# Kernel optimization log

Measured on AMD Instinct MI355X. Metric: run time of the kernel, lower is better.

Reference implementation:

```python
import jax, jax.numpy as jnp
import numpy as np

NUM_HEAD = 8


def setup_inputs() -> dict:
    key = jax.random.key(0)
    ks = jax.random.split(key, 8)
    B, N, M, C, R = 4, 2048, 2048, 256, 128
    s = 1.0 / np.sqrt(C)
    return {
        "input_q": jax.random.normal(ks[0], (B, N, C), jnp.float32),
        "input_k": jax.random.normal(ks[1], (B, M, C), jnp.float32),
        "input_v": jax.random.normal(ks[2], (B, M, C), jnp.float32),
        "rpe_indices": jax.random.randint(ks[3], (B, N, M), 0, R, jnp.int32),
        "key_masks": jnp.zeros((B, M), jnp.float32),
        "Wq": jax.random.normal(ks[4], (C, C), jnp.float32) * s,
        "bq": jnp.zeros((C,), jnp.float32),
        "Wk": jax.random.normal(ks[5], (C, C), jnp.float32) * s,
        "bk": jnp.zeros((C,), jnp.float32),
        "Wv": jax.random.normal(ks[6], (C, C), jnp.float32) * s,
        "bv": jnp.zeros((C,), jnp.float32),
        "rpe_bank": jax.random.normal(ks[7], (R, C), jnp.float32),
    }


def reference(input_q, input_k, input_v, rpe_indices, key_masks,
              Wq, bq, Wk, bk, Wv, bv, rpe_bank):
    B, N, C = input_q.shape
    M = input_k.shape[1]
    H = NUM_HEAD
    Dh = C // H
    R = rpe_bank.shape[0]

    # projections -> (B, H, len, Dh)
    q = (input_q @ Wq + bq).reshape(B, N, H, Dh).transpose(0, 2, 1, 3)
    k = (input_k @ Wk + bk).reshape(B, M, H, Dh).transpose(0, 2, 1, 3)
    v = (input_v @ Wv + bv).reshape(B, M, H, Dh).transpose(0, 2, 1, 3)

    # RPE bank split per head: (H, R, Dh)
    rpe = rpe_bank.reshape(R, H, Dh).transpose(1, 0, 2)

    # q . rpe for all bins, then gather per (n, m) relative index
    scores_p_all = jnp.einsum('bhnd,hrd->bhnr', q, rpe)            # (B,H,N,R)
    idx = jnp.broadcast_to(rpe_indices[:, None, :, :], (B, H, N, M))
    scores_p = jnp.take_along_axis(scores_p_all, idx, axis=-1)     # (B,H,N,M)

    scores_e = jnp.einsum('bhnd,bhmd->bhnm', q, k)                 # (B,H,N,M)
    scores = (scores_e + scores_p) / jnp.sqrt(jnp.asarray(Dh, q.dtype))
    scores = scores + key_masks[:, None, None, :]

    attn = jax.nn.softmax(scores, axis=-1)
    out = jnp.einsum('bhnm,bhmd->bhnd', attn, v)                   # (B,H,N,Dh)
    return out.transpose(0, 2, 1, 3).reshape(B, N, C)
```

## Files before the change

kernel.cpp:

```cpp
#include <hip/hip_runtime.h>
#include <hip/hip_bf16.h>

#define B_ 4
#define N_ 2048
#define M_ 2048
#define C_ 256
#define H_ 8
#define DH_ 32
#define R_ 128

typedef __bf16 bf16x8 __attribute__((ext_vector_type(8)));
typedef float f32x4 __attribute__((ext_vector_type(4)));

__global__ __launch_bounds__(256) void wtrans_kernel(
    const float* __restrict__ Wq, const float* __restrict__ Wk,
    const float* __restrict__ Wv, __bf16* __restrict__ out)
{
    __shared__ float t[32][33];
    int pz = blockIdx.z;
    const float* W = pz == 0 ? Wq : (pz == 1 ? Wk : Wv);
    int j0 = blockIdx.x * 32, k0 = blockIdx.y * 32;
    int tx = threadIdx.x, ty = threadIdx.y;
#pragma unroll
    for (int i = 0; i < 4; ++i)
        t[ty + 8 * i][tx] = W[(k0 + ty + 8 * i) * C_ + j0 + tx];
    __syncthreads();
    __bf16* o = out + (size_t)pz * C_ * C_;
#pragma unroll
    for (int i = 0; i < 4; ++i)
        o[(j0 + ty + 8 * i) * C_ + k0 + tx] = (__bf16)t[tx][ty + 8 * i];
}

__global__ __launch_bounds__(256) void proj_kernel(
    const float* __restrict__ Xq, const float* __restrict__ Xk, const float* __restrict__ Xv,
    const float* __restrict__ bq, const float* __restrict__ bk, const float* __restrict__ bv,
    const __bf16* __restrict__ Wt,
    __bf16* __restrict__ qb, __bf16* __restrict__ kb, __bf16* __restrict__ vt)
{
    int pz = blockIdx.z;
    const float* X = pz == 0 ? Xq : (pz == 1 ? Xk : Xv);
    const float* bias = pz == 0 ? bq : (pz == 1 ? bk : bv);
    const __bf16* W = Wt + (size_t)pz * C_ * C_;

    int r0 = blockIdx.x * 64, c0 = blockIdx.y * 64;
    int w = threadIdx.x >> 6, lane = threadIdx.x & 63;
    int lg = lane >> 4, lr = lane & 15;
    int rw = r0 + w * 16;

    f32x4 z = {0.f, 0.f, 0.f, 0.f};
    f32x4 acc[4] = {z, z, z, z};

    for (int ks = 0; ks < 8; ++ks) {
        const float* ap = X + (size_t)(rw + lr) * C_ + ks * 32 + lg * 8;
        float4 a0 = *(const float4*)ap;
        float4 a1 = *(const float4*)(ap + 4);
        bf16x8 af;
        af[0] = (__bf16)a0.x; af[1] = (__bf16)a0.y; af[2] = (__bf16)a0.z; af[3] = (__bf16)a0.w;
        af[4] = (__bf16)a1.x; af[5] = (__bf16)a1.y; af[6] = (__bf16)a1.z; af[7] = (__bf16)a1.w;
#pragma unroll
        for (int ns = 0; ns < 4; ++ns) {
            bf16x8 bfv = *(const bf16x8*)(W + (size_t)(c0 + ns * 16 + lr) * C_ + ks * 32 + lg * 8);
            acc[ns] = __builtin_amdgcn_mfma_f32_16x16x32_bf16(af, bfv, acc[ns], 0, 0, 0);
        }
    }

#pragma unroll
    for (int ns = 0; ns < 4; ++ns) {
        int j = c0 + ns * 16 + lr;
        float bj = bias[j];
        int h = j >> 5, d = j & 31;
#pragma unroll
        for (int reg = 0; reg < 4; ++reg) {
            int r = rw + lg * 4 + reg;
            int bb = r >> 11, n = r & (N_ - 1);
            float val = acc[ns][reg] + bj;
            if (pz == 0)
                qb[(((size_t)bb * H_ + h) * N_ + n) * DH_ + d] = (__bf16)val;
            else if (pz == 1)
                kb[(((size_t)bb * H_ + h) * M_ + n) * DH_ + d] = (__bf16)val;
            else
                vt[(((size_t)bb * H_ + h) * DH_ + d) * M_ + n] = (__bf16)val;
        }
    }
}

__global__ __launch_bounds__(512) void attn_kernel(
    const __bf16* __restrict__ qb, const __bf16* __restrict__ kb,
    const __bf16* __restrict__ vt, const int* __restrict__ ridx,
    const float* __restrict__ kmask, const float* __restrict__ rbank,
    float* __restrict__ out)
{
    __shared__ int idxS[16][66];
    __shared__ __bf16 Pall[H_][16][R_];
    __shared__ __bf16 Pt[H_][1024];

    int b = blockIdx.y;
    int n0 = blockIdx.x * 16;
    int h = threadIdx.x >> 6, lane = threadIdx.x & 63;
    int lg = lane >> 4, lr = lane & 15;

    f32x4 z = {0.f, 0.f, 0.f, 0.f};

    bf16x8 qf = *(const bf16x8*)(qb + (((size_t)b * H_ + h) * N_ + n0 + lr) * DH_ + lg * 8);

    for (int rs = 0; rs < R_ / 16; ++rs) {
        const float* rp = rbank + (size_t)(rs * 16 + lr) * C_ + h * DH_ + lg * 8;
        float4 r0v = *(const float4*)rp;
        float4 r1v = *(const float4*)(rp + 4);
        bf16x8 rf;
        rf[0] = (__bf16)r0v.x; rf[1] = (__bf16)r0v.y; rf[2] = (__bf16)r0v.z; rf[3] = (__bf16)r0v.w;
        rf[4] = (__bf16)r1v.x; rf[5] = (__bf16)r1v.y; rf[6] = (__bf16)r1v.z; rf[7] = (__bf16)r1v.w;
        f32x4 pc = __builtin_amdgcn_mfma_f32_16x16x32_bf16(qf, rf, z, 0, 0, 0);
#pragma unroll
        for (int reg = 0; reg < 4; ++reg)
            Pall[h][lg * 4 + reg][rs * 16 + lr] = (__bf16)pc[reg];
    }

    const float scale = 0.17677669529663687f;
    float mrun[4], lrun[4];
    f32x4 acc[2] = {z, z};
#pragma unroll
    for (int r = 0; r < 4; ++r) { mrun[r] = -1e30f; lrun[r] = 0.f; }

    const __bf16* Kh = kb + ((size_t)b * H_ + h) * M_ * DH_;
    const __bf16* Vh = vt + ((size_t)b * H_ + h) * DH_ * M_;
    const float* km = kmask + (size_t)b * M_;
    const int* ixb = ridx + ((size_t)b * N_ + n0) * M_;
    char* ptb = (char*)&Pt[h][0];

    for (int mt = 0; mt < M_ / 64; ++mt) {
        int m0 = mt * 64;
        __syncthreads();
        {
            int t = threadIdx.x;
            int row = t >> 5, c = (t & 31) * 2;
            int2 iv = *(const int2*)(ixb + (size_t)row * M_ + m0 + c);
            idxS[row][c] = iv.x; idxS[row][c + 1] = iv.y;
        }
        __syncthreads();

        f32x4 s[4];
#pragma unroll
        for (int ms = 0; ms < 4; ++ms) {
            bf16x8 kf = *(const bf16x8*)(Kh + (size_t)(m0 + ms * 16 + lr) * DH_ + lg * 8);
            s[ms] = __builtin_amdgcn_mfma_f32_16x16x32_bf16(qf, kf, z, 0, 0, 0);
        }

        float sv[4][4];
#pragma unroll
        for (int ms = 0; ms < 4; ++ms) {
            int ml = ms * 16 + lr;
            float mk = km[m0 + ml];
#pragma unroll
            for (int reg = 0; reg < 4; ++reg) {
                int n = lg * 4 + reg;
                int i = idxS[n][ml];
                float p = (float)Pall[h][n][i];
                sv[ms][reg] = (s[ms][reg] + p) * scale + mk;
            }
        }

        float pq[4][4];
#pragma unroll
        for (int reg = 0; reg < 4; ++reg) {
            float mx = fmaxf(fmaxf(sv[0][reg], sv[1][reg]), fmaxf(sv[2][reg], sv[3][reg]));
#pragma unroll
            for (int off = 1; off < 16; off <<= 1)
                mx = fmaxf(mx, __shfl_xor(mx, off, 16));
            float mnew = fmaxf(mrun[reg], mx);
            float alpha = __expf(mrun[reg] - mnew);
            float sum = 0.f;
#pragma unroll
            for (int ms = 0; ms < 4; ++ms) {
                float p = __expf(sv[ms][reg] - mnew);
                pq[ms][reg] = p; sum += p;
            }
#pragma unroll
            for (int off = 1; off < 16; off <<= 1)
                sum += __shfl_xor(sum, off, 16);
            lrun[reg] = lrun[reg] * alpha + sum;
            mrun[reg] = mnew;
            acc[0][reg] *= alpha;
            acc[1][reg] *= alpha;
        }

#pragma unroll
        for (int ms = 0; ms < 4; ++ms) {
#pragma unroll
            for (int reg = 0; reg < 4; ++reg) {
                int n = lg * 4 + reg;
                int byteoff = ((n * 64 + ms * 16 + lr) * 2) ^ ((n & 7) << 4);
                *(__bf16*)(ptb + byteoff) = (__bf16)pq[ms][reg];
            }
        }

#pragma unroll
        for (int ks = 0; ks < 2; ++ks) {
            int byteoff = ((lr * 64 + ks * 32 + lg * 8) * 2) ^ ((lr & 7) << 4);
            bf16x8 pf = *(const bf16x8*)(ptb + byteoff);
#pragma unroll
            for (int ds = 0; ds < 2; ++ds) {
                bf16x8 vf = *(const bf16x8*)(Vh + (size_t)(ds * 16 + lr) * M_ + m0 + ks * 32 + lg * 8);
                acc[ds] = __builtin_amdgcn_mfma_f32_16x16x32_bf16(pf, vf, acc[ds], 0, 0, 0);
            }
        }
    }

#pragma unroll
    for (int ds = 0; ds < 2; ++ds) {
#pragma unroll
        for (int reg = 0; reg < 4; ++reg) {
            int n = lg * 4 + reg;
            out[((size_t)b * N_ + n0 + n) * C_ + h * DH_ + ds * 16 + lr] =
                acc[ds][reg] / lrun[reg];
        }
    }
}

extern "C" void kernel_launch(void* const* d_in, const int* in_sizes, int n_in,
                              void* d_out, int out_size, void* d_ws, size_t ws_size,
                              hipStream_t stream) {
    const float* Xq = (const float*)d_in[0];
    const float* Xk = (const float*)d_in[1];
    const float* Xv = (const float*)d_in[2];
    const int* ridx = (const int*)d_in[3];
    const float* kmask = (const float*)d_in[4];
    const float* Wq = (const float*)d_in[5];
    const float* bq = (const float*)d_in[6];
    const float* Wk = (const float*)d_in[7];
    const float* bk = (const float*)d_in[8];
    const float* Wv = (const float*)d_in[9];
    const float* bv = (const float*)d_in[10];
    const float* rbank = (const float*)d_in[11];
    float* outp = (float*)d_out;

    char* ws = (char*)d_ws;
    __bf16* Wt = (__bf16*)ws;
    __bf16* qb = (__bf16*)(ws + 393216);
    __bf16* kb = (__bf16*)(ws + 393216 + 4194304);
    __bf16* vt = (__bf16*)(ws + 393216 + 8388608);

    wtrans_kernel<<<dim3(8, 8, 3), dim3(32, 8), 0, stream>>>(Wq, Wk, Wv, Wt);
    proj_kernel<<<dim3(128, 4, 3), 256, 0, stream>>>(Xq, Xk, Xv, bq, bk, bv, Wt, qb, kb, vt);
    attn_kernel<<<dim3(N_ / 16, B_), 512, 0, stream>>>(qb, kb, vt, ridx, kmask, rbank, outp);
}
```

Baseline: 162.3 us.

## Restructure attention: transposed scores, register-prefetched indices, lazy rescale, wider projection tiles

```diff
diff --git a/kernel.cpp b/kernel.cpp
--- a/kernel.cpp
+++ b/kernel.cpp
@@ -42,13 +42,15 @@
     const float* bias = pz == 0 ? bq : (pz == 1 ? bk : bv);
     const __bf16* W = Wt + (size_t)pz * C_ * C_;
 
-    int r0 = blockIdx.x * 64, c0 = blockIdx.y * 64;
+    int r0 = blockIdx.x * 64;
     int w = threadIdx.x >> 6, lane = threadIdx.x & 63;
     int lg = lane >> 4, lr = lane & 15;
     int rw = r0 + w * 16;
 
     f32x4 z = {0.f, 0.f, 0.f, 0.f};
-    f32x4 acc[4] = {z, z, z, z};
+    f32x4 acc[16];
+#pragma unroll
+    for (int ns = 0; ns < 16; ++ns) acc[ns] = z;
 
     for (int ks = 0; ks < 8; ++ks) {
         const float* ap = X + (size_t)(rw + lr) * C_ + ks * 32 + lg * 8;
@@ -58,47 +60,67 @@
         af[0] = (__bf16)a0.x; af[1] = (__bf16)a0.y; af[2] = (__bf16)a0.z; af[3] = (__bf16)a0.w;
         af[4] = (__bf16)a1.x; af[5] = (__bf16)a1.y; af[6] = (__bf16)a1.z; af[7] = (__bf16)a1.w;
 #pragma unroll
-        for (int ns = 0; ns < 4; ++ns) {
-            bf16x8 bfv = *(const bf16x8*)(W + (size_t)(c0 + ns * 16 + lr) * C_ + ks * 32 + lg * 8);
+        for (int ns = 0; ns < 16; ++ns) {
+            bf16x8 bfv = *(const bf16x8*)(W + (size_t)(ns * 16 + lr) * C_ + ks * 32 + lg * 8);
             acc[ns] = __builtin_amdgcn_mfma_f32_16x16x32_bf16(af, bfv, acc[ns], 0, 0, 0);
         }
     }
 
-#pragma unroll
-    for (int ns = 0; ns < 4; ++ns) {
-        int j = c0 + ns * 16 + lr;
-        float bj = bias[j];
-        int h = j >> 5, d = j & 31;
-#pragma unroll
-        for (int reg = 0; reg < 4; ++reg) {
-            int r = rw + lg * 4 + reg;
-            int bb = r >> 11, n = r & (N_ - 1);
-            float val = acc[ns][reg] + bj;
-            if (pz == 0)
-                qb[(((size_t)bb * H_ + h) * N_ + n) * DH_ + d] = (__bf16)val;
-            else if (pz == 1)
-                kb[(((size_t)bb * H_ + h) * M_ + n) * DH_ + d] = (__bf16)val;
-            else
-                vt[(((size_t)bb * H_ + h) * DH_ + d) * M_ + n] = (__bf16)val;
-        }
-    }
-}
-
-__global__ __launch_bounds__(512) void attn_kernel(
+    if (pz < 2) {
+#pragma unroll
+        for (int ns = 0; ns < 16; ++ns) {
+            int j = ns * 16 + lr;
+            float bj = bias[j];
+            int h = j >> 5, d = j & 31;
+#pragma unroll
+            for (int reg = 0; reg < 4; ++reg) {
+                int r = rw + lg * 4 + reg;
+                int bb = r >> 11, n = r & (N_ - 1);
+                float val = acc[ns][reg] + bj;
+                if (pz == 0)
+                    qb[(((size_t)bb * H_ + h) * N_ + n) * DH_ + d] = (__bf16)val;
+                else
+                    kb[(((size_t)bb * H_ + h) * M_ + n) * DH_ + d] = (__bf16)val;
+            }
+        }
+    } else {
+        int r = rw + lg * 4;
+        int bb = r >> 11, n = r & (N_ - 1);
+#pragma unroll
+        for (int ns = 0; ns < 16; ++ns) {
+            int j = ns * 16 + lr;
+            float bj = bias[j];
+            int h = j >> 5, d = j & 31;
+            ushort4 pk;
+            __bf16 t0 = (__bf16)(acc[ns][0] + bj);
+            __bf16 t1 = (__bf16)(acc[ns][1] + bj);
+            __bf16 t2 = (__bf16)(acc[ns][2] + bj);
+            __bf16 t3 = (__bf16)(acc[ns][3] + bj);
+            pk.x = __builtin_bit_cast(unsigned short, t0);
+            pk.y = __builtin_bit_cast(unsigned short, t1);
+            pk.z = __builtin_bit_cast(unsigned short, t2);
+            pk.w = __builtin_bit_cast(unsigned short, t3);
+            *(ushort4*)((unsigned short*)vt + (((size_t)bb * H_ + h) * DH_ + d) * M_ + n) = pk;
+        }
+    }
+}
+
+__global__ __launch_bounds__(512, 4) void attn_kernel(
     const __bf16* __restrict__ qb, const __bf16* __restrict__ kb,
     const __bf16* __restrict__ vt, const int* __restrict__ ridx,
     const float* __restrict__ kmask, const float* __restrict__ rbank,
     float* __restrict__ out)
 {
-    __shared__ int idxS[16][66];
     __shared__ __bf16 Pall[H_][16][R_];
-    __shared__ __bf16 Pt[H_][1024];
-
-    int b = blockIdx.y;
-    int n0 = blockIdx.x * 16;
+    __shared__ unsigned int Pt[H_][512];
+
+    int lin = blockIdx.x;
+    int b = (lin & 7) >> 1;
+    int xq = ((lin >> 3) << 1) | (lin & 1);
+    int n0 = xq * 16;
+
     int h = threadIdx.x >> 6, lane = threadIdx.x & 63;
     int lg = lane >> 4, lr = lane & 15;
-
     f32x4 z = {0.f, 0.f, 0.f, 0.f};
 
     bf16x8 qf = *(const bf16x8*)(qb + (((size_t)b * H_ + h) * N_ + n0 + lr) * DH_ + lg * 8);
@@ -115,105 +137,128 @@
         for (int reg = 0; reg < 4; ++reg)
             Pall[h][lg * 4 + reg][rs * 16 + lr] = (__bf16)pc[reg];
     }
+    __syncthreads();
 
     const float scale = 0.17677669529663687f;
-    float mrun[4], lrun[4];
-    f32x4 acc[2] = {z, z};
-#pragma unroll
-    for (int r = 0; r < 4; ++r) { mrun[r] = -1e30f; lrun[r] = 0.f; }
-
     const __bf16* Kh = kb + ((size_t)b * H_ + h) * M_ * DH_;
     const __bf16* Vh = vt + ((size_t)b * H_ + h) * DH_ * M_;
     const float* km = kmask + (size_t)b * M_;
-    const int* ixb = ridx + ((size_t)b * N_ + n0) * M_;
-    char* ptb = (char*)&Pt[h][0];
+    const int* ixr = ridx + ((size_t)b * N_ + n0 + lr) * M_ + 4 * lg;
+    unsigned int* Ptw = &Pt[h][0];
+    const __bf16* PallR = &Pall[h][lr][0];
+    int swz = (lr & 7) << 2;
+
+    float mrow = -1e30f, lrun = 0.f;
+    f32x4 acc[2] = {z, z};
+
+    int4 ixc[4];
+#pragma unroll
+    for (int ms = 0; ms < 4; ++ms) ixc[ms] = *(const int4*)(ixr + 16 * ms);
 
     for (int mt = 0; mt < M_ / 64; ++mt) {
         int m0 = mt * 64;
-        __syncthreads();
-        {
-            int t = threadIdx.x;
-            int row = t >> 5, c = (t & 31) * 2;
-            int2 iv = *(const int2*)(ixb + (size_t)row * M_ + m0 + c);
-            idxS[row][c] = iv.x; idxS[row][c + 1] = iv.y;
-        }
-        __syncthreads();
-
-        f32x4 s[4];
+
+        int pm = (mt < 31) ? m0 + 64 : 0;
+        int4 ixn[4];
+#pragma unroll
+        for (int ms = 0; ms < 4; ++ms) ixn[ms] = *(const int4*)(ixr + pm + 16 * ms);
+
+        bf16x8 kf[4];
+#pragma unroll
+        for (int ms = 0; ms < 4; ++ms)
+            kf[ms] = *(const bf16x8*)(Kh + (size_t)(m0 + ms * 16 + lr) * DH_ + lg * 8);
+
+        float pg[16];
 #pragma unroll
         for (int ms = 0; ms < 4; ++ms) {
-            bf16x8 kf = *(const bf16x8*)(Kh + (size_t)(m0 + ms * 16 + lr) * DH_ + lg * 8);
-            s[ms] = __builtin_amdgcn_mfma_f32_16x16x32_bf16(qf, kf, z, 0, 0, 0);
-        }
-
-        float sv[4][4];
+            pg[ms * 4 + 0] = (float)PallR[ixc[ms].x];
+            pg[ms * 4 + 1] = (float)PallR[ixc[ms].y];
+            pg[ms * 4 + 2] = (float)PallR[ixc[ms].z];
+            pg[ms * 4 + 3] = (float)PallR[ixc[ms].w];
+        }
+
+        float4 mk[4];
+#pragma unroll
+        for (int ms = 0; ms < 4; ++ms)
+            mk[ms] = *(const float4*)(km + m0 + ms * 16 + 4 * lg);
+
+        f32x4 st[4];
+#pragma unroll
+        for (int ms = 0; ms < 4; ++ms)
+            st[ms] = __builtin_amdgcn_mfma_f32_16x16x32_bf16(kf[ms], qf, z, 0, 0, 0);
+
+        float sv[16];
 #pragma unroll
         for (int ms = 0; ms < 4; ++ms) {
-            int ml = ms * 16 + lr;
-            float mk = km[m0 + ml];
+            sv[ms * 4 + 0] = (st[ms][0] + pg[ms * 4 + 0]) * scale + mk[ms].x;
+            sv[ms * 4 + 1] = (st[ms][1] + pg[ms * 4 + 1]) * scale + mk[ms].y;
+            sv[ms * 4 + 2] = (st[ms][2] + pg[ms * 4 + 2]) * scale + mk[ms].z;
+            sv[ms * 4 + 3] = (st[ms][3] + pg[ms * 4 + 3]) * scale + mk[ms].w;
+        }
+
+        float pmax = sv[0];
+#pragma unroll
+        for (int j = 1; j < 16; ++j) pmax = fmaxf(pmax, sv[j]);
+        pmax = fmaxf(pmax, __shfl_xor(pmax, 16));
+        pmax = fmaxf(pmax, __shfl_xor(pmax, 32));
+
+        if (!__all(pmax - mrow <= 8.0f)) {
+            float mnew = fmaxf(mrow, pmax);
+            float alpha = __expf(mrow - mnew);
+            mrow = mnew;
+            lrun *= alpha;
 #pragma unroll
             for (int reg = 0; reg < 4; ++reg) {
-                int n = lg * 4 + reg;
-                int i = idxS[n][ml];
-                float p = (float)Pall[h][n][i];
-                sv[ms][reg] = (s[ms][reg] + p) * scale + mk;
-            }
-        }
-
-        float pq[4][4];
-#pragma unroll
-        for (int reg = 0; reg < 4; ++reg) {
-            float mx = fmaxf(fmaxf(sv[0][reg], sv[1][reg]), fmaxf(sv[2][reg], sv[3][reg]));
-#pragma unroll
-            for (int off = 1; off < 16; off <<= 1)
-                mx = fmaxf(mx, __shfl_xor(mx, off, 16));
-            float mnew = fmaxf(mrun[reg], mx);
-            float alpha = __expf(mrun[reg] - mnew);
-            float sum = 0.f;
-#pragma unroll
-            for (int ms = 0; ms < 4; ++ms) {
-                float p = __expf(sv[ms][reg] - mnew);
-                pq[ms][reg] = p; sum += p;
-            }
-#pragma unroll
-            for (int off = 1; off < 16; off <<= 1)
-                sum += __shfl_xor(sum, off, 16);
-            lrun[reg] = lrun[reg] * alpha + sum;
-            mrun[reg] = mnew;
-            acc[0][reg] *= alpha;
-            acc[1][reg] *= alpha;
-        }
+                float aB = __shfl(alpha, lg * 4 + reg);
+                acc[0][reg] *= aB;
+                acc[1][reg] *= aB;
+            }
+        }
+
+        float pq[16], ssum = 0.f;
+#pragma unroll
+        for (int j = 0; j < 16; ++j) {
+            pq[j] = __expf(sv[j] - mrow);
+            ssum += pq[j];
+        }
+        ssum += __shfl_xor(ssum, 16);
+        ssum += __shfl_xor(ssum, 32);
+        lrun += ssum;
 
 #pragma unroll
         for (int ms = 0; ms < 4; ++ms) {
 #pragma unroll
-            for (int reg = 0; reg < 4; ++reg) {
-                int n = lg * 4 + reg;
-                int byteoff = ((n * 64 + ms * 16 + lr) * 2) ^ ((n & 7) << 4);
-                *(__bf16*)(ptb + byteoff) = (__bf16)pq[ms][reg];
-            }
-        }
+            for (int j = 0; j < 2; ++j) {
+                __bf16 lo = (__bf16)pq[ms * 4 + 2 * j];
+                __bf16 hi = (__bf16)pq[ms * 4 + 2 * j + 1];
+                unsigned int wv = (unsigned int)__builtin_bit_cast(unsigned short, lo) |
+                                  ((unsigned int)__builtin_bit_cast(unsigned short, hi) << 16);
+                Ptw[lr * 32 + ((ms * 8 + lg * 2 + j) ^ swz)] = wv;
+            }
+        }
+        asm volatile("s_waitcnt lgkmcnt(0)" ::: "memory");
 
 #pragma unroll
         for (int ks = 0; ks < 2; ++ks) {
-            int byteoff = ((lr * 64 + ks * 32 + lg * 8) * 2) ^ ((lr & 7) << 4);
-            bf16x8 pf = *(const bf16x8*)(ptb + byteoff);
+            bf16x8 pf = *(const bf16x8*)(&Ptw[lr * 32 + ((ks * 16 + lg * 4) ^ swz)]);
 #pragma unroll
             for (int ds = 0; ds < 2; ++ds) {
                 bf16x8 vf = *(const bf16x8*)(Vh + (size_t)(ds * 16 + lr) * M_ + m0 + ks * 32 + lg * 8);
                 acc[ds] = __builtin_amdgcn_mfma_f32_16x16x32_bf16(pf, vf, acc[ds], 0, 0, 0);
             }
         }
-    }
-
-#pragma unroll
-    for (int ds = 0; ds < 2; ++ds) {
-#pragma unroll
-        for (int reg = 0; reg < 4; ++reg) {
-            int n = lg * 4 + reg;
-            out[((size_t)b * N_ + n0 + n) * C_ + h * DH_ + ds * 16 + lr] =
-                acc[ds][reg] / lrun[reg];
-        }
+
+#pragma unroll
+        for (int ms = 0; ms < 4; ++ms) ixc[ms] = ixn[ms];
+    }
+
+#pragma unroll
+    for (int reg = 0; reg < 4; ++reg) {
+        float lB = __shfl(lrun, lg * 4 + reg);
+        float inv = 1.0f / lB;
+        size_t rb = ((size_t)b * N_ + n0 + lg * 4 + reg) * C_ + h * DH_;
+        out[rb + lr] = acc[0][reg] * inv;
+        out[rb + 16 + lr] = acc[1][reg] * inv;
     }
 }
 
@@ -241,6 +286,6 @@
     __bf16* vt = (__bf16*)(ws + 393216 + 8388608);
 
     wtrans_kernel<<<dim3(8, 8, 3), dim3(32, 8), 0, stream>>>(Wq, Wk, Wv, Wt);
-    proj_kernel<<<dim3(128, 4, 3), 256, 0, stream>>>(Xq, Xk, Xv, bq, bk, bv, Wt, qb, kb, vt);
-    attn_kernel<<<dim3(N_ / 16, B_), 512, 0, stream>>>(qb, kb, vt, ridx, kmask, rbank, outp);
-}
+    proj_kernel<<<dim3(128, 1, 3), 256, 0, stream>>>(Xq, Xk, Xv, bq, bk, bv, Wt, qb, kb, vt);
+    attn_kernel<<<512, 512, 0, stream>>>(qb, kb, vt, ridx, kmask, rbank, outp);
+}
```

Result: slower. 210.8 us (+29.9%).
